# Kernel optimization log

Hardware: AMD Instinct MI355X
Metric: run time of the kernel (lower is better)

The kernel has to match this reference:

```python
import jax, jax.numpy as jnp
import numpy as np

N_NODES = 100000
N_EDGES = 1600000
N_GRAPHS = 512
IN_DIM = 128
HID = 128


def setup_inputs() -> dict:
    key = jax.random.key(0)
    ks = jax.random.split(key, 8)
    x = jax.random.normal(ks[0], (N_NODES, IN_DIM), dtype=jnp.float32)
    edge_index = jax.random.randint(ks[1], (2, N_EDGES), 0, N_NODES, dtype=jnp.int64)
    batch = jnp.sort(jax.random.randint(ks[2], (N_NODES,), 0, N_GRAPHS, dtype=jnp.int64))
    s1 = 1.0 / np.sqrt(IN_DIM)
    s2 = 1.0 / np.sqrt(HID)
    W1 = jax.random.normal(ks[3], (IN_DIM, HID), dtype=jnp.float32) * s1
    b1 = jnp.zeros((HID,), dtype=jnp.float32)
    W2 = jax.random.normal(ks[4], (HID, HID), dtype=jnp.float32) * s2
    b2 = jnp.zeros((HID,), dtype=jnp.float32)
    Wp = jax.random.normal(ks[5], (HID, 1), dtype=jnp.float32) * s2
    bp = jnp.zeros((1,), dtype=jnp.float32)
    return {"x": x, "edge_index": edge_index, "batch": batch,
            "W1": W1, "b1": b1, "W2": W2, "b2": b2, "Wp": Wp, "bp": bp}


def _gcn_conv(x, W, b, src, dst, deg_inv_sqrt):
    # PyG GCNConv: linear transform, then normalized scatter-add (self-loops
    # already appended to src/dst), then bias.
    h = x @ W                                   # [N, H]
    norm = deg_inv_sqrt[src] * deg_inv_sqrt[dst]  # [E+N]
    msg = h[src] * norm[:, None]                # gather + scale
    out = jax.ops.segment_sum(msg, dst, num_segments=N_NODES)
    return out + b


def reference(x, edge_index, batch, W1, b1, W2, b2, Wp, bp):
    # Add self-loops once; degree (with self-loops) over target nodes.
    si = jnp.arange(N_NODES, dtype=edge_index.dtype)
    src = jnp.concatenate([edge_index[0], si])
    dst = jnp.concatenate([edge_index[1], si])
    ones = jnp.ones(src.shape[0], dtype=x.dtype)
    deg = jax.ops.segment_sum(ones, dst, num_segments=N_NODES)
    deg_inv_sqrt = jnp.where(deg > 0, jax.lax.rsqrt(jnp.maximum(deg, 1.0)), 0.0)

    h = jax.nn.relu(_gcn_conv(x, W1, b1, src, dst, deg_inv_sqrt))  # dropout = identity (eval)
    h = jax.nn.relu(_gcn_conv(h, W2, b2, src, dst, deg_inv_sqrt))

    # global_mean_pool over graph ids
    sums = jax.ops.segment_sum(h, batch, num_segments=N_GRAPHS)
    cnts = jax.ops.segment_sum(jnp.ones(N_NODES, dtype=h.dtype), batch, num_segments=N_GRAPHS)
    pooled = sums / jnp.maximum(cnts, 1.0)[:, None]               # [G, H]

    return (pooled @ Wp + bp).squeeze(-1)                          # [G]
```

## Files before the change

kernel.cpp:

```cpp
#include <hip/hip_runtime.h>
#include <hip/hip_bf16.h>

#define NN 100000
#define NG 512
#define H  128

typedef _Float16 half8 __attribute__((ext_vector_type(8)));
typedef _Float16 half4v __attribute__((ext_vector_type(4)));

__global__ __launch_bounds__(256) void k_hist(const int* __restrict__ dst,
                                              int* __restrict__ deg, int E) {
    int e = blockIdx.x * 256 + threadIdx.x;
    if (e < E) atomicAdd(&deg[dst[e]], 1);
}

__global__ __launch_bounds__(256) void k_scan_block(const int* __restrict__ deg,
                                                    int* __restrict__ rowptr,
                                                    int* __restrict__ bsum, int n) {
    __shared__ int s[256];
    int tid = threadIdx.x;
    int i = blockIdx.x * 256 + tid;
    int v = (i < n) ? deg[i] : 0;
    s[tid] = v;
    __syncthreads();
    #pragma unroll
    for (int off = 1; off < 256; off <<= 1) {
        int t = (tid >= off) ? s[tid - off] : 0;
        __syncthreads();
        s[tid] += t;
        __syncthreads();
    }
    if (i < n) rowptr[i] = s[tid] - v;
    if (tid == 255) bsum[blockIdx.x] = s[255];
}

__global__ __launch_bounds__(512) void k_scan_top(int* __restrict__ bsum, int nb) {
    __shared__ int s[512];
    int tid = threadIdx.x;
    int v = (tid < nb) ? bsum[tid] : 0;
    s[tid] = v;
    __syncthreads();
    #pragma unroll
    for (int off = 1; off < 512; off <<= 1) {
        int t = (tid >= off) ? s[tid - off] : 0;
        __syncthreads();
        s[tid] += t;
        __syncthreads();
    }
    if (tid < nb) bsum[tid] = s[tid] - v;
}

__global__ __launch_bounds__(256) void k_scan_fin(int* __restrict__ rowptr,
                                                  const int* __restrict__ bsum,
                                                  const int* __restrict__ deg,
                                                  int* __restrict__ cursor,
                                                  float* __restrict__ dinv,
                                                  int n, int E) {
    int i = blockIdx.x * 256 + threadIdx.x;
    if (i >= n) return;
    int r = rowptr[i] + bsum[i >> 8];
    rowptr[i] = r;
    cursor[i] = r;
    dinv[i] = rsqrtf((float)deg[i] + 1.0f);
    if (i == 0) rowptr[n] = E;
}

__global__ __launch_bounds__(256) void k_fill(const int* __restrict__ src,
                                              const int* __restrict__ dst,
                                              int* __restrict__ cursor,
                                              int* __restrict__ col, int E) {
    int e = blockIdx.x * 256 + threadIdx.x;
    if (e >= E) return;
    int d = dst[e];
    int pos = atomicAdd(&cursor[d], 1);
    col[pos] = src[e];
}

__global__ __launch_bounds__(256) void k_sortrows(const int* __restrict__ rowptr,
                                                  int* __restrict__ col, int n) {
    int node = blockIdx.x * 4 + (threadIdx.x >> 6);
    int lane = threadIdx.x & 63;
    if (node >= n) return;
    int e0 = rowptr[node], end = rowptr[node + 1];
    int deg = end - e0;
    if (deg <= 1 || deg > 64) return;
    int v = (lane < deg) ? col[e0 + lane] : 0x7fffffff;
    #pragma unroll
    for (int k = 2; k <= 64; k <<= 1) {
        #pragma unroll
        for (int j = k >> 1; j > 0; j >>= 1) {
            int p = __shfl_xor(v, j);
            bool up = ((lane & k) == 0);
            bool keepmin = (((lane & j) == 0) == up);
            v = keepmin ? min(v, p) : max(v, p);
        }
    }
    if (lane < deg) col[e0 + lane] = v;
}

__global__ __launch_bounds__(256) void gemm128h(const float* __restrict__ A,
                                                const float* __restrict__ W,
                                                const float* __restrict__ scale,
                                                _Float16* __restrict__ C) {
    __shared__ float xs[32][64];
    __shared__ float ws[64][128];
    const int tid = threadIdx.x;
    const int row0 = blockIdx.x * 32;
    const int tx = tid & 31;
    const int ty = tid >> 5;
    float acc[4][4] = {};

    for (int kc = 0; kc < 128; kc += 64) {
        #pragma unroll
        for (int i = tid; i < 32 * 16; i += 256) {
            int r = i >> 4, k4 = i & 15;
            ((float4*)xs[r])[k4] =
                ((const float4*)(A + (size_t)(row0 + r) * H + kc))[k4];
        }
        #pragma unroll
        for (int i = tid; i < 64 * 32; i += 256) {
            int k = i >> 5, c4 = i & 31;
            ((float4*)ws[k])[c4] = ((const float4*)(W + (size_t)(kc + k) * H))[c4];
        }
        __syncthreads();
        #pragma unroll
        for (int k = 0; k < 64; ++k) {
            float4 wv = ((float4*)ws[k])[tx];
            float xv[4];
            #pragma unroll
            for (int r = 0; r < 4; ++r) xv[r] = xs[4 * ty + r][k];
            #pragma unroll
            for (int r = 0; r < 4; ++r) {
                acc[r][0] += xv[r] * wv.x;
                acc[r][1] += xv[r] * wv.y;
                acc[r][2] += xv[r] * wv.z;
                acc[r][3] += xv[r] * wv.w;
            }
        }
        __syncthreads();
    }
    #pragma unroll
    for (int r = 0; r < 4; ++r) {
        int row = row0 + 4 * ty + r;
        float sc = scale[row];
        half4v v;
        v[0] = (_Float16)(acc[r][0] * sc);
        v[1] = (_Float16)(acc[r][1] * sc);
        v[2] = (_Float16)(acc[r][2] * sc);
        v[3] = (_Float16)(acc[r][3] * sc);
        ((half4v*)(C + (size_t)row * H))[tx] = v;
    }
}

__device__ __forceinline__ void gather_rows_h(const half8* __restrict__ t8,
                                              const int* __restrict__ col,
                                              int node, int e0, int end,
                                              float acc[8]) {
    const int lane = threadIdx.x & 63;
    const int q = lane >> 4;
    const int l16 = lane & 15;
    float a0[8] = {}, a1[8] = {};
    if (q == 0) {
        half8 v = t8[(size_t)node * 16 + l16];
        #pragma unroll
        for (int i = 0; i < 8; ++i) a0[i] = (float)v[i];
    }
    for (int base = e0; base < end; base += 64) {
        int ce = base + lane;
        int cidx = (ce < end) ? col[ce] : 0;
        int m = min(64, end - base);
        int nf = m >> 2;
        int g = 0;
        for (; g + 2 <= nf; g += 2) {
            int s0 = __shfl(cidx, 4 * g + q);
            int s1 = __shfl(cidx, 4 * g + 4 + q);
            half8 v0 = t8[(size_t)s0 * 16 + l16];
            half8 v1 = t8[(size_t)s1 * 16 + l16];
            #pragma unroll
            for (int i = 0; i < 8; ++i) {
                a0[i] += (float)v0[i];
                a1[i] += (float)v1[i];
            }
        }
        if (g < nf) {
            int s0 = __shfl(cidx, 4 * g + q);
            half8 v0 = t8[(size_t)s0 * 16 + l16];
            #pragma unroll
            for (int i = 0; i < 8; ++i) a0[i] += (float)v0[i];
        }
        int tail = m & 3;
        if (tail) {
            int s = __shfl(cidx, 4 * nf + q);
            if (q < tail) {
                half8 v = t8[(size_t)s * 16 + l16];
                #pragma unroll
                for (int i = 0; i < 8; ++i) a0[i] += (float)v[i];
            }
        }
    }
    #pragma unroll
    for (int i = 0; i < 8; ++i) {
        float t = a0[i] + a1[i];
        t += __shfl_xor(t, 16);
        t += __shfl_xor(t, 32);
        acc[i] = t;
    }
}

__global__ __launch_bounds__(256) void k_gather1(const _Float16* __restrict__ tS,
                                                 const int* __restrict__ rowptr,
                                                 const int* __restrict__ col,
                                                 const float* __restrict__ dinv,
                                                 const float* __restrict__ b,
                                                 float* __restrict__ out, int n) {
    int node = blockIdx.x * 4 + (threadIdx.x >> 6);
    int lane = threadIdx.x & 63;
    int q = lane >> 4, l16 = lane & 15;
    if (node >= n) return;
    int e0 = rowptr[node], end = rowptr[node + 1];
    float acc[8];
    gather_rows_h((const half8*)tS, col, node, e0, end, acc);
    if (q == 0) {
        float dn = dinv[node];
        const float4* b4 = (const float4*)b;
        float4 bb0 = b4[2 * l16], bb1 = b4[2 * l16 + 1];
        float4 r0, r1;
        r0.x = fmaxf(dn * acc[0] + bb0.x, 0.0f);
        r0.y = fmaxf(dn * acc[1] + bb0.y, 0.0f);
        r0.z = fmaxf(dn * acc[2] + bb0.z, 0.0f);
        r0.w = fmaxf(dn * acc[3] + bb0.w, 0.0f);
        r1.x = fmaxf(dn * acc[4] + bb1.x, 0.0f);
        r1.y = fmaxf(dn * acc[5] + bb1.y, 0.0f);
        r1.z = fmaxf(dn * acc[6] + bb1.z, 0.0f);
        r1.w = fmaxf(dn * acc[7] + bb1.w, 0.0f);
        float4* o = (float4*)(out + (size_t)node * H + l16 * 8);
        o[0] = r0;
        o[1] = r1;
    }
}

__global__ __launch_bounds__(256) void k_gather2(const _Float16* __restrict__ tS,
                                                 const int* __restrict__ rowptr,
                                                 const int* __restrict__ col,
                                                 const float* __restrict__ dinv,
                                                 const float* __restrict__ b,
                                                 const float* __restrict__ Wp,
                                                 const int* __restrict__ batch,
                                                 float* __restrict__ pool,
                                                 float* __restrict__ cnt, int n) {
    int node = blockIdx.x * 4 + (threadIdx.x >> 6);
    int lane = threadIdx.x & 63;
    int l16 = lane & 15;
    if (node >= n) return;
    int e0 = rowptr[node], end = rowptr[node + 1];
    float acc[8];
    gather_rows_h((const half8*)tS, col, node, e0, end, acc);
    float dn = dinv[node];
    const float4* b4 = (const float4*)b;
    const float4* w4 = (const float4*)Wp;
    float4 bb0 = b4[2 * l16], bb1 = b4[2 * l16 + 1];
    float4 wp0 = w4[2 * l16], wp1 = w4[2 * l16 + 1];
    float s = fmaxf(dn * acc[0] + bb0.x, 0.0f) * wp0.x +
              fmaxf(dn * acc[1] + bb0.y, 0.0f) * wp0.y +
              fmaxf(dn * acc[2] + bb0.z, 0.0f) * wp0.z +
              fmaxf(dn * acc[3] + bb0.w, 0.0f) * wp0.w +
              fmaxf(dn * acc[4] + bb1.x, 0.0f) * wp1.x +
              fmaxf(dn * acc[5] + bb1.y, 0.0f) * wp1.y +
              fmaxf(dn * acc[6] + bb1.z, 0.0f) * wp1.z +
              fmaxf(dn * acc[7] + bb1.w, 0.0f) * wp1.w;
    s += __shfl_xor(s, 1);
    s += __shfl_xor(s, 2);
    s += __shfl_xor(s, 4);
    s += __shfl_xor(s, 8);
    if (lane == 0) {
        int g = batch[node];
        atomicAdd(&pool[g], s);
        atomicAdd(&cnt[g], 1.0f);
    }
}

__global__ __launch_bounds__(256) void final_out_kernel(const float* __restrict__ pool,
                                                        const float* __restrict__ cnt,
                                                        const float* __restrict__ bp,
                                                        float* __restrict__ out, int g) {
    int i = blockIdx.x * 256 + threadIdx.x;
    if (i < g) out[i] = pool[i] / fmaxf(cnt[i], 1.0f) + bp[0];
}

extern "C" void kernel_launch(void* const* d_in, const int* in_sizes, int n_in,
                              void* d_out, int out_size, void* d_ws, size_t ws_size,
                              hipStream_t stream) {
    const float* x     = (const float*)d_in[0];
    const int*   ei    = (const int*)d_in[1];
    const int*   batch = (const int*)d_in[2];
    const float* W1    = (const float*)d_in[3];
    const float* b1    = (const float*)d_in[4];
    const float* W2    = (const float*)d_in[5];
    const float* b2    = (const float*)d_in[6];
    const float* Wp    = (const float*)d_in[7];
    const float* bp    = (const float*)d_in[8];
    float* out = (float*)d_out;

    const int E = in_sizes[1] / 2;
    const int* src = ei;
    const int* dst = ei + E;

    const size_t BUFH = (size_t)NN * H * sizeof(_Float16);
    const size_t BUFF = (size_t)NN * H * sizeof(float);
    const size_t NI  = 401408;
    char* ws = (char*)d_ws;
    size_t off = 0;
    _Float16* tS  = (_Float16*)(ws + off); off += BUFH;
    float* h1     = (float*)(ws + off); off += BUFF;
    int*   deg    = (int*)  (ws + off); off += NI;
    int*   rowptr = (int*)  (ws + off); off += NI;
    int*   cursor = (int*)  (ws + off); off += NI;
    float* dinv   = (float*)(ws + off); off += NI;
    int*   col    = (int*)  (ws + off); off += ((size_t)E * 4 + 4095) / 4096 * 4096;
    int*   bsum   = (int*)  (ws + off); off += 4096;
    float* pool   = (float*)(ws + off); off += 2048;
    float* cnt    = (float*)(ws + off); off += 2048;

    const int NB = (NN + 255) / 256;

    hipMemsetAsync(deg, 0, NN * sizeof(int), stream);
    hipMemsetAsync(pool, 0, 4096, stream);
    k_hist<<<(E + 255) / 256, 256, 0, stream>>>(dst, deg, E);
    k_scan_block<<<NB, 256, 0, stream>>>(deg, rowptr, bsum, NN);
    k_scan_top<<<1, 512, 0, stream>>>(bsum, NB);
    k_scan_fin<<<NB, 256, 0, stream>>>(rowptr, bsum, deg, cursor, dinv, NN, E);
    k_fill<<<(E + 255) / 256, 256, 0, stream>>>(src, dst, cursor, col, E);
    k_sortrows<<<(NN + 3) / 4, 256, 0, stream>>>(rowptr, col, NN);

    gemm128h<<<NN / 32, 256, 0, stream>>>(x, W1, dinv, tS);
    k_gather1<<<(NN + 3) / 4, 256, 0, stream>>>(tS, rowptr, col, dinv, b1, h1, NN);

    gemm128h<<<NN / 32, 256, 0, stream>>>(h1, W2, dinv, tS);
    k_gather2<<<(NN + 3) / 4, 256, 0, stream>>>(tS, rowptr, col, dinv, b2, Wp,
                                                batch, pool, cnt, NN);

    final_out_kernel<<<(NG + 255) / 256, 256, 0, stream>>>(pool, cnt, bp, out, NG);
}
```

Measured before the change: 746.6 us.

## Replace FP32 SIMT GEMM with FP16 MFMA GEMM and store h1 in half

Replaces the scalar FP32 tiled GEMM with an MFMA 16x16x32 f16 kernel that stages A and a transposed fp16 copy of W in padded LDS. x is first converted to fp16 by a separate kernel, and the layer-1 gather now writes h1 as fp16, which halves its write and read traffic. This cuts GEMM arithmetic cost and activation bandwidth. In exchange it adds a conversion pass, reduces input precision to fp16, and makes each block re-transpose W into LDS.

```diff
diff --git a/kernel.cpp b/kernel.cpp
--- a/kernel.cpp
+++ b/kernel.cpp
@@ -7,6 +7,7 @@
 
 typedef _Float16 half8 __attribute__((ext_vector_type(8)));
 typedef _Float16 half4v __attribute__((ext_vector_type(4)));
+typedef float f32x4 __attribute__((ext_vector_type(4)));
 
 __global__ __launch_bounds__(256) void k_hist(const int* __restrict__ dst,
                                               int* __restrict__ deg, int E) {
@@ -98,57 +99,77 @@
     if (lane < deg) col[e0 + lane] = v;
 }
 
-__global__ __launch_bounds__(256) void gemm128h(const float* __restrict__ A,
-                                                const float* __restrict__ W,
-                                                const float* __restrict__ scale,
-                                                _Float16* __restrict__ C) {
-    __shared__ float xs[32][64];
-    __shared__ float ws[64][128];
+__global__ __launch_bounds__(256) void k_cvt_h(const float* __restrict__ in,
+                                               _Float16* __restrict__ out, int n4) {
+    int i = blockIdx.x * 256 + threadIdx.x;
+    if (i >= n4) return;
+    float4 v = ((const float4*)in)[i];
+    half4v h;
+    h[0] = (_Float16)v.x;
+    h[1] = (_Float16)v.y;
+    h[2] = (_Float16)v.z;
+    h[3] = (_Float16)v.w;
+    ((half4v*)out)[i] = h;
+}
+
+#define LDA 136
+__global__ __launch_bounds__(256) void gemm_mfma(const _Float16* __restrict__ A,
+                                                 const float* __restrict__ W,
+                                                 const float* __restrict__ scale,
+                                                 _Float16* __restrict__ C, int n) {
+    __shared__ _Float16 As[64 * LDA];
+    __shared__ _Float16 Wt[128 * LDA];
     const int tid = threadIdx.x;
-    const int row0 = blockIdx.x * 32;
-    const int tx = tid & 31;
-    const int ty = tid >> 5;
-    float acc[4][4] = {};
-
-    for (int kc = 0; kc < 128; kc += 64) {
+    const int row0 = blockIdx.x * 64;
+
+    #pragma unroll
+    for (int i = 0; i < 4; ++i) {
+        int f = i * 256 + tid;
+        int r = f >> 4, c8 = f & 15;
+        int gr = row0 + r;
+        half8 v;
         #pragma unroll
-        for (int i = tid; i < 32 * 16; i += 256) {
-            int r = i >> 4, k4 = i & 15;
-            ((float4*)xs[r])[k4] =
-                ((const float4*)(A + (size_t)(row0 + r) * H + kc))[k4];
-        }
+        for (int j = 0; j < 8; ++j) v[j] = (_Float16)0.0f;
+        if (gr < n) v = ((const half8*)(A + (size_t)gr * H))[c8];
+        *((half8*)(As + r * LDA + c8 * 8)) = v;
+    }
+    #pragma unroll
+    for (int i = 0; i < 16; ++i) {
+        int f = i * 256 + tid;
+        int k = f >> 5, c4 = f & 31;
+        float4 v = ((const float4*)(W + (size_t)k * H))[c4];
+        Wt[(c4 * 4 + 0) * LDA + k] = (_Float16)v.x;
+        Wt[(c4 * 4 + 1) * LDA + k] = (_Float16)v.y;
+        Wt[(c4 * 4 + 2) * LDA + k] = (_Float16)v.z;
+        Wt[(c4 * 4 + 3) * LDA + k] = (_Float16)v.w;
+    }
+    __syncthreads();
+
+    const int w = tid >> 6;
+    const int lane = tid & 63;
+    const int l16 = lane & 15, quad = lane >> 4;
+    f32x4 acc[8] = {};
+    const _Float16* aBase = As + (w * 16 + l16) * LDA + quad * 8;
+    const _Float16* bBase = Wt + l16 * LDA + quad * 8;
+    #pragma unroll
+    for (int kk = 0; kk < 4; ++kk) {
+        half8 af = *((const half8*)(aBase + kk * 32));
         #pragma unroll
-        for (int i = tid; i < 64 * 32; i += 256) {
-            int k = i >> 5, c4 = i & 31;
-            ((float4*)ws[k])[c4] = ((const float4*)(W + (size_t)(kc + k) * H))[c4];
-        }
-        __syncthreads();
-        #pragma unroll
-        for (int k = 0; k < 64; ++k) {
-            float4 wv = ((float4*)ws[k])[tx];
-            float xv[4];
+        for (int nt = 0; nt < 8; ++nt) {
+            half8 bf = *((const half8*)(bBase + nt * 16 * LDA + kk * 32));
+            acc[nt] = __builtin_amdgcn_mfma_f32_16x16x32_f16(af, bf, acc[nt], 0, 0, 0);
+        }
+    }
+    #pragma unroll
+    for (int r = 0; r < 4; ++r) {
+        int R = row0 + w * 16 + quad * 4 + r;
+        if (R < n) {
+            float sc = scale[R];
+            _Float16* crow = C + (size_t)R * H + l16;
             #pragma unroll
-            for (int r = 0; r < 4; ++r) xv[r] = xs[4 * ty + r][k];
-            #pragma unroll
-            for (int r = 0; r < 4; ++r) {
-                acc[r][0] += xv[r] * wv.x;
-                acc[r][1] += xv[r] * wv.y;
-                acc[r][2] += xv[r] * wv.z;
-                acc[r][3] += xv[r] * wv.w;
-            }
-        }
-        __syncthreads();
-    }
-    #pragma unroll
-    for (int r = 0; r < 4; ++r) {
-        int row = row0 + 4 * ty + r;
-        float sc = scale[row];
-        half4v v;
-        v[0] = (_Float16)(acc[r][0] * sc);
-        v[1] = (_Float16)(acc[r][1] * sc);
-        v[2] = (_Float16)(acc[r][2] * sc);
-        v[3] = (_Float16)(acc[r][3] * sc);
-        ((half4v*)(C + (size_t)row * H))[tx] = v;
+            for (int nt = 0; nt < 8; ++nt)
+                crow[nt * 16] = (_Float16)(acc[nt][r] * sc);
+        }
     }
 }
 
@@ -212,7 +233,7 @@
                                                  const int* __restrict__ col,
                                                  const float* __restrict__ dinv,
                                                  const float* __restrict__ b,
-                                                 float* __restrict__ out, int n) {
+                                                 _Float16* __restrict__ out, int n) {
     int node = blockIdx.x * 4 + (threadIdx.x >> 6);
     int lane = threadIdx.x & 63;
     int q = lane >> 4, l16 = lane & 15;
@@ -224,18 +245,16 @@
         float dn = dinv[node];
         const float4* b4 = (const float4*)b;
         float4 bb0 = b4[2 * l16], bb1 = b4[2 * l16 + 1];
-        float4 r0, r1;
-        r0.x = fmaxf(dn * acc[0] + bb0.x, 0.0f);
-        r0.y = fmaxf(dn * acc[1] + bb0.y, 0.0f);
-        r0.z = fmaxf(dn * acc[2] + bb0.z, 0.0f);
-        r0.w = fmaxf(dn * acc[3] + bb0.w, 0.0f);
-        r1.x = fmaxf(dn * acc[4] + bb1.x, 0.0f);
-        r1.y = fmaxf(dn * acc[5] + bb1.y, 0.0f);
-        r1.z = fmaxf(dn * acc[6] + bb1.z, 0.0f);
-        r1.w = fmaxf(dn * acc[7] + bb1.w, 0.0f);
-        float4* o = (float4*)(out + (size_t)node * H + l16 * 8);
-        o[0] = r0;
-        o[1] = r1;
+        half8 hv;
+        hv[0] = (_Float16)fmaxf(dn * acc[0] + bb0.x, 0.0f);
+        hv[1] = (_Float16)fmaxf(dn * acc[1] + bb0.y, 0.0f);
+        hv[2] = (_Float16)fmaxf(dn * acc[2] + bb0.z, 0.0f);
+        hv[3] = (_Float16)fmaxf(dn * acc[3] + bb0.w, 0.0f);
+        hv[4] = (_Float16)fmaxf(dn * acc[4] + bb1.x, 0.0f);
+        hv[5] = (_Float16)fmaxf(dn * acc[5] + bb1.y, 0.0f);
+        hv[6] = (_Float16)fmaxf(dn * acc[6] + bb1.z, 0.0f);
+        hv[7] = (_Float16)fmaxf(dn * acc[7] + bb1.w, 0.0f);
+        ((half8*)out)[(size_t)node * 16 + l16] = hv;
     }
 }
 
@@ -306,12 +325,12 @@
     const int* dst = ei + E;
 
     const size_t BUFH = (size_t)NN * H * sizeof(_Float16);
-    const size_t BUFF = (size_t)NN * H * sizeof(float);
     const size_t NI  = 401408;
     char* ws = (char*)d_ws;
     size_t off = 0;
     _Float16* tS  = (_Float16*)(ws + off); off += BUFH;
-    float* h1     = (float*)(ws + off); off += BUFF;
+    _Float16* h1  = (_Float16*)(ws + off); off += BUFH;
+    _Float16* xh  = (_Float16*)(ws + off); off += BUFH;
     int*   deg    = (int*)  (ws + off); off += NI;
     int*   rowptr = (int*)  (ws + off); off += NI;
     int*   cursor = (int*)  (ws + off); off += NI;
@@ -332,10 +351,12 @@
     k_fill<<<(E + 255) / 256, 256, 0, stream>>>(src, dst, cursor, col, E);
     k_sortrows<<<(NN + 3) / 4, 256, 0, stream>>>(rowptr, col, NN);
 
-    gemm128h<<<NN / 32, 256, 0, stream>>>(x, W1, dinv, tS);
+    k_cvt_h<<<(NN * 32 + 255) / 256, 256, 0, stream>>>(x, xh, NN * 32);
+
+    gemm_mfma<<<(NN + 63) / 64, 256, 0, stream>>>(xh, W1, dinv, tS, NN);
     k_gather1<<<(NN + 3) / 4, 256, 0, stream>>>(tS, rowptr, col, dinv, b1, h1, NN);
 
-    gemm128h<<<NN / 32, 256, 0, stream>>>(h1, W2, dinv, tS);
+    gemm_mfma<<<(NN + 63) / 64, 256, 0, stream>>>(h1, W2, dinv, tS, NN);
     k_gather2<<<(NN + 3) / 4, 256, 0, stream>>>(tS, rowptr, col, dinv, b2, Wp,
                                                 batch, pool, cnt, NN);
 
```

New measurement: 704.6 us. 5.6% less time.
